# Optimization experiments

Measured on AMD Instinct MI355X. Metric: run time of the kernel, lower is better.

## Reference

```python
import jax, jax.numpy as jnp
import numpy as np

EPS = 1e-8
SMOOTH = 9.0   # lambda_softmax
STEPS = 3      # iteration_step
SLOPE = 0.1    # LeakyReLU slope used by clipped_l2norm


def l2norm(x, axis=-1):
    # matches torch l2norm: x / (sqrt(sum x^2) + eps)
    return x / (jnp.sqrt(jnp.sum(x * x, axis=axis, keepdims=True)) + EPS)


def cos_sim(a, b, axis=-1):
    num = jnp.sum(a * b, axis=axis)
    den = jnp.linalg.norm(a, axis=axis) * jnp.linalg.norm(b, axis=axis)
    return num / jnp.maximum(den, EPS)


def duplicate_mask(cap):
    # same_word logic: cap_k identical to cap_c (off-diagonal). Computed via
    # pairwise squared distances (one GEMM) instead of O(B^2 L d) direct compare.
    B = cap.shape[0]
    flat = cap.reshape(B, -1)
    sq = jnp.sum(flat * flat, axis=1)
    d2 = sq[:, None] + sq[None, :] - 2.0 * (flat @ flat.T)
    return (d2 <= 1e-6) & (~jnp.eye(B, dtype=bool))


def gated(q, a, Wl, bl, Wg, bg):
    cat = jnp.concatenate([q, a], axis=-1)            # (..., 2d)
    lin = jnp.tanh(cat @ Wl.T + bl)
    gate = jax.nn.sigmoid(cat @ Wg.T + bg)
    return q * gate + lin * (1.0 - gate)


def imram_forward(img, cap, W_lt2i, b_lt2i, W_gt2i, b_gt2i,
                  W_li2t, b_li2t, W_gi2t, b_gi2t):
    B, R, D = img.shape
    L = cap.shape[1]
    dup = duplicate_mask(cap)                         # symmetric
    total = jnp.zeros((B, B), img.dtype)              # [caption, image] (training=True transpose)

    # ---- text-to-image: query = caption words, context = image regions ----
    cap_e = jnp.broadcast_to(cap[:, None], (B, B, L, D))   # (cap c, img i, L, D)
    q = cap_e
    for _ in range(STEPS):
        attn = jnp.einsum('ird,cild->cirl', img, q)          # (c,i,R,L)
        attn = l2norm(jax.nn.leaky_relu(attn, SLOPE), axis=-1)   # clipped_l2norm over queryL
        attn = jax.nn.softmax(SMOOTH * attn, axis=2)             # softmax over source regions r
        wc = jnp.einsum('cirl,ird->cild', attn, img)             # weightedContext (c,i,L,D)
        sim = jnp.mean(cos_sim(cap_e, wc, axis=-1), axis=-1)    # (c,i)
        total = total + jnp.where(dup, -1.0, sim)
        q = l2norm(gated(q, wc, W_lt2i, b_lt2i, W_gt2i, b_gt2i), axis=-1)

    # ---- image-to-text: query = image regions, context = caption words ----
    img_e = jnp.broadcast_to(img[None], (B, B, R, D))
    q = img_e
    for _ in range(STEPS):
        attn = jnp.einsum('cld,cird->cilr', cap, q)          # (c,i,L,R)
        attn = l2norm(jax.nn.leaky_relu(attn, SLOPE), axis=-1)   # over queryL (= R)
        attn = jax.nn.softmax(SMOOTH * attn, axis=2)             # over source words l
        wc = jnp.einsum('cilr,cld->cird', attn, cap)             # (c,i,R,D)
        sim = jnp.mean(cos_sim(img_e, wc, axis=-1), axis=-1)
        total = total + jnp.where(dup, -1.0, sim)
        q = l2norm(gated(q, wc, W_li2t, b_li2t, W_gi2t, b_gi2t), axis=-1)

    return total


def setup_inputs() -> dict:
    key = jax.random.key(0)
    ks = jax.random.split(key, 8)
    B, R, L, D = 32, 36, 40, 1024
    img_emb = jax.random.normal(ks[0], (B, R, D), dtype=jnp.float32)
    cap_emb = jax.random.normal(ks[1], (B, L, D), dtype=jnp.float32)
    cap_lens = jax.random.randint(ks[2], (B,), 5, L + 1)
    s = 0.02
    W_lt2i = s * jax.random.normal(ks[3], (D, 2 * D), dtype=jnp.float32)
    W_gt2i = s * jax.random.normal(ks[4], (D, 2 * D), dtype=jnp.float32)
    W_li2t = s * jax.random.normal(ks[5], (D, 2 * D), dtype=jnp.float32)
    W_gi2t = s * jax.random.normal(ks[6], (D, 2 * D), dtype=jnp.float32)
    z = jnp.zeros((D,), jnp.float32)
    return {
        'img_emb': img_emb, 'cap_emb': cap_emb,
        'W_lt2i': W_lt2i, 'b_lt2i': z, 'W_gt2i': W_gt2i, 'b_gt2i': z,
        'W_li2t': W_li2t, 'b_li2t': z, 'W_gi2t': W_gi2t, 'b_gi2t': z,
        'cap_lens': cap_lens,
    }


def reference(img_emb, cap_emb, W_lt2i, b_lt2i, W_gt2i, b_gt2i,
              W_li2t, b_li2t, W_gi2t, b_gi2t, cap_lens):
    # cap_lens is read but never used by the original forward (n_word unused)
    return imram_forward(img_emb, cap_emb, W_lt2i, b_lt2i, W_gt2i, b_gt2i,
                         W_li2t, b_li2t, W_gi2t, b_gi2t)
```

## Files before the change

### kernel.cpp

```cpp
#include <hip/hip_runtime.h>
#include <stdint.h>
#include <math.h>

typedef unsigned short u16;
typedef unsigned int u32;

#define EPSF 1e-8f
#define SMOOTHF 9.0f
#define SLOPEF 0.1f

__device__ __forceinline__ u16 f2bf(float f) {
  union { float f; u32 u; } v; v.f = f;
  u32 u = v.u;
  u32 r = (u + 0x7FFFu + ((u >> 16) & 1u)) >> 16;
  return (u16)r;
}
__device__ __forceinline__ float bf2f(u16 h) {
  union { u32 u; float f; } v; v.u = ((u32)h) << 16;
  return v.f;
}

__device__ __forceinline__ float wave_red_sum(float x) {
#pragma unroll
  for (int off = 32; off; off >>= 1) x += __shfl_xor(x, off, 64);
  return x;
}

__device__ __forceinline__ float block_red_sum(float x) {
  __shared__ float rs[4];
  x = wave_red_sum(x);
  const int lane = threadIdx.x & 63, wv = threadIdx.x >> 6;
  if (lane == 0) rs[wv] = x;
  __syncthreads();
  float r = rs[0] + rs[1] + rs[2] + rs[3];
  __syncthreads();
  return r;
}

__global__ __launch_bounds__(256) void rownorm_kernel(
    const float* __restrict__ cap, const float* __restrict__ img,
    float* __restrict__ capn, float* __restrict__ imgn) {
  const int row = blockIdx.x;
  const float* p; float* o;
  if (row < 1280) { p = cap + (size_t)row * 1024; o = capn + row; }
  else            { p = img + (size_t)(row - 1280) * 1024; o = imgn + (row - 1280); }
  float ss = 0.f;
  for (int d = threadIdx.x; d < 1024; d += 256) { float v = p[d]; ss += v * v; }
  float t = block_red_sum(ss);
  if (threadIdx.x == 0) *o = sqrtf(t);
}

__global__ __launch_bounds__(256) void dup_kernel(
    const float* __restrict__ cap, int* __restrict__ dup) {
  const int b = blockIdx.x;
  const int c = b >> 5, i = b & 31;
  float ss = 0.f;
  if (c != i) {
    const float* A = cap + (size_t)c * 40960;
    const float* B = cap + (size_t)i * 40960;
    for (int e = threadIdx.x; e < 40960; e += 256) { float d = A[e] - B[e]; ss += d * d; }
  }
  float t = block_red_sum(ss);
  if (threadIdx.x == 0) dup[b] = (c != i && t <= 1e-6f) ? 1 : 0;
}

__global__ __launch_bounds__(256) void wconv_kernel(
    const float* __restrict__ Wl, const float* __restrict__ Wg, u16* __restrict__ out) {
  const size_t idx = ((size_t)blockIdx.x * 256 + threadIdx.x) * 4;
  const int n = (int)(idx >> 11);
  const int k = (int)(idx & 2047);
  const float* src = (n & 1) ? &Wg[(size_t)(n >> 1) * 2048 + k] : &Wl[(size_t)(n >> 1) * 2048 + k];
  float4 v = *(const float4*)src;
  ushort4 o;
  o.x = f2bf(v.x); o.y = f2bf(v.y); o.z = f2bf(v.z); o.w = f2bf(v.w);
  *(ushort4*)&out[idx] = o;
}

__global__ __launch_bounds__(256) void bfpad_kernel(
    const float* __restrict__ src, u16* __restrict__ dst, int nrows) {
  const int b = blockIdx.x;
  const int blk = b / 48, r = b - blk * 48;
  u16* orow = dst + (size_t)b * 1024;
  const int tid = threadIdx.x;
  ushort4 o = {0, 0, 0, 0};
  if (r < nrows) {
    const float4 v = *(const float4*)&src[((size_t)blk * nrows + r) * 1024 + tid * 4];
    o.x = f2bf(v.x); o.y = f2bf(v.y); o.z = f2bf(v.z); o.w = f2bf(v.w);
  }
  *(ushort4*)&orow[tid * 4] = o;
}

__global__ __launch_bounds__(256) void ss_kernel(
    const float* __restrict__ src, float* __restrict__ out, int nrows) {
  const int s = blockIdx.x, b = blockIdx.y;
  float* orow = out + ((size_t)b * 48 + s) * 64;
  __shared__ float Ls[1024];
  const int tid = threadIdx.x;
  if (s < nrows)
    *(float4*)&Ls[tid * 4] = *(const float4*)&src[((size_t)b * nrows + s) * 1024 + tid * 4];
  __syncthreads();
  const int s2 = tid >> 2, koff = (tid & 3) * 256;
  float acc = 0.f;
  if (s < nrows && s2 < nrows) {
    const float* r2 = src + ((size_t)b * nrows + s2) * 1024 + koff;
    for (int k = 0; k < 256; k += 4) {
      float4 a = *(const float4*)&Ls[koff + k];
      float4 bb = *(const float4*)&r2[k];
      acc += a.x * bb.x + a.y * bb.y + a.z * bb.z + a.w * bb.w;
    }
  }
  acc += __shfl_xor(acc, 1, 64);
  acc += __shfl_xor(acc, 2, 64);
  if ((tid & 3) == 0) orow[s2] = acc;
}

typedef short bf16x8 __attribute__((ext_vector_type(8)));
typedef float f32x4 __attribute__((ext_vector_type(4)));

#define GLDS(gp, lp)                                                                   \
  __builtin_amdgcn_global_load_lds((const __attribute__((address_space(1))) void*)(gp), \
                                   (__attribute__((address_space(3))) void*)(lp), 16, 0, 0)

__global__ __launch_bounds__(256) void gemm_flex_kernel(
    const u16* __restrict__ A, const u16* __restrict__ B, u16* __restrict__ Cout,
    int koff, int trans) {
  __shared__ u16 As[128 * 32];
  __shared__ u16 Bs[128 * 32];
  const int tid = threadIdx.x;
  const int lane = tid & 63;
  const int wave = tid >> 6;
  const int wm = (wave >> 1) * 64;
  const int wn = (wave & 1) * 64;
  const int bm = blockIdx.x * 128;
  const int bn = blockIdx.y * 128;
  const int lr = lane & 15;
  const int lq = lane >> 4;
  f32x4 acc[4][4] = {};
  const int e0 = tid * 8;
  const int r0 = e0 >> 5;
  const int c0 = e0 & 31;
  const u16* Ag0 = A + (size_t)(bm + r0) * 1024 + c0;
  const u16* Ag1 = A + (size_t)(bm + r0 + 64) * 1024 + c0;
  const u16* Bg0 = B + (size_t)(bn + r0) * 2048 + koff + c0;
  const u16* Bg1 = B + (size_t)(bn + r0 + 64) * 2048 + koff + c0;
  u16* As0 = As + e0; u16* As1 = As + e0 + 2048;
  u16* Bs0 = Bs + e0; u16* Bs1 = Bs + e0 + 2048;
  for (int k0 = 0; k0 < 1024; k0 += 32) {
    GLDS(Ag0 + k0, As0);
    GLDS(Ag1 + k0, As1);
    GLDS(Bg0 + k0, Bs0);
    GLDS(Bg1 + k0, Bs1);
    __syncthreads();
    bf16x8 af[4], bfr[4];
#pragma unroll
    for (int mi = 0; mi < 4; mi++)
      af[mi] = *(const bf16x8*)&As[(wm + mi * 16 + lr) * 32 + lq * 8];
#pragma unroll
    for (int ni = 0; ni < 4; ni++)
      bfr[ni] = *(const bf16x8*)&Bs[(wn + ni * 16 + lr) * 32 + lq * 8];
#pragma unroll
    for (int mi = 0; mi < 4; mi++)
#pragma unroll
      for (int ni = 0; ni < 4; ni++)
        acc[mi][ni] = __builtin_amdgcn_mfma_f32_16x16x32_bf16(af[mi], bfr[ni], acc[mi][ni], 0, 0, 0);
    __syncthreads();
  }
#pragma unroll
  for (int mi = 0; mi < 4; mi++) {
#pragma unroll
    for (int ni = 0; ni < 4; ni++) {
      const int col = bn + wn + ni * 16 + lr;
      const int rowb = bm + wm + mi * 16 + lq * 4;
      if (!trans) {
#pragma unroll
        for (int r = 0; r < 4; r++)
          Cout[(size_t)(rowb + r) * 2048 + col] = f2bf(acc[mi][ni][r]);
      } else {
#pragma unroll
        for (int r = 0; r < 4; r++) {
          const int m = rowb + r;
          const int blk = m / 48, s = m - blk * 48;
          Cout[((size_t)blk * 2048 + col) * 64 + s] = f2bf(acc[mi][ni][r]);
        }
      }
    }
  }
}

__global__ __launch_bounds__(256) void gemm_e_kernel(
    const u16* __restrict__ A, const u16* __restrict__ B, float* __restrict__ C) {
  __shared__ u16 As[128 * 32];
  __shared__ u16 Bs[128 * 32];
  const int tid = threadIdx.x;
  const int lane = tid & 63;
  const int wave = tid >> 6;
  const int wm = (wave >> 1) * 64;
  const int wn = (wave & 1) * 64;
  const int bm = blockIdx.x * 128;
  const int bn = blockIdx.y * 128;
  const int lr = lane & 15;
  const int lq = lane >> 4;
  f32x4 acc[4][4] = {};
  const int e0 = tid * 8;
  const int r0 = e0 >> 5;
  const int c0 = e0 & 31;
  const u16* Ag0 = A + (size_t)(bm + r0) * 1024 + c0;
  const u16* Ag1 = A + (size_t)(bm + r0 + 64) * 1024 + c0;
  const u16* Bg0 = B + (size_t)(bn + r0) * 1024 + c0;
  const u16* Bg1 = B + (size_t)(bn + r0 + 64) * 1024 + c0;
  u16* As0 = As + e0; u16* As1 = As + e0 + 2048;
  u16* Bs0 = Bs + e0; u16* Bs1 = Bs + e0 + 2048;
  for (int k0 = 0; k0 < 1024; k0 += 32) {
    GLDS(Ag0 + k0, As0);
    GLDS(Ag1 + k0, As1);
    GLDS(Bg0 + k0, Bs0);
    GLDS(Bg1 + k0, Bs1);
    __syncthreads();
    bf16x8 af[4], bfr[4];
#pragma unroll
    for (int mi = 0; mi < 4; mi++)
      af[mi] = *(const bf16x8*)&As[(wm + mi * 16 + lr) * 32 + lq * 8];
#pragma unroll
    for (int ni = 0; ni < 4; ni++)
      bfr[ni] = *(const bf16x8*)&Bs[(wn + ni * 16 + lr) * 32 + lq * 8];
#pragma unroll
    for (int mi = 0; mi < 4; mi++)
#pragma unroll
      for (int ni = 0; ni < 4; ni++)
        acc[mi][ni] = __builtin_amdgcn_mfma_f32_16x16x32_bf16(af[mi], bfr[ni], acc[mi][ni], 0, 0, 0);
    __syncthreads();
  }
#pragma unroll
  for (int mi = 0; mi < 4; mi++)
#pragma unroll
    for (int ni = 0; ni < 4; ni++) {
      const int col = bn + wn + ni * 16 + lr;
      const int rowb = bm + wm + mi * 16 + lq * 4;
#pragma unroll
      for (int r = 0; r < 4; r++)
        C[(size_t)(rowb + r) * 1536 + col] = acc[mi][ni][r];
    }
}

template <int STEP, int NQ, int BM>
__global__ __launch_bounds__(512) void wcgate_kernel(
    const u16* __restrict__ attnTg, const u16* __restrict__ q2nd,
    const u16* __restrict__ qref, const u16* __restrict__ SWT,
    const u16* __restrict__ Wcat, const u16* __restrict__ qw0,
    const float* __restrict__ bl, const float* __restrict__ bg,
    u16* __restrict__ Uout, int p0, int swz) {
  constexpr int NT = (STEP == 1) ? 17 : 1;
  constexpr int BUF = (BM + 256) * 64;
  constexpr int WMR = BM / 32;
  constexpr int APASS = BM / 64;
  constexpr int QPASS = BM / 32;
  __shared__ u16 sh[(STEP == 0) ? 73728 : 2 * BUF];
  const int tid = threadIdx.x;
  const int lane = tid & 63;
  const int wave = tid >> 6;
  const int wr = wave >> 2, wc = wave & 3;
  const int wm = wr * (BM / 2), wn = wc * 64;
  const int lr = lane & 15, lq = lane >> 4;
  const int b = blockIdx.y * 8 + blockIdx.x;
  int bmi, bni;
  if (swz) { bmi = (b & 7) + (b >> 6) * 8; bni = (b >> 3) & 7; }
  else     { bmi = blockIdx.y; bni = blockIdx.x; }
  const int bm = bmi * BM;
  const int bn = bni * 256;
  const int sIdx = (p0 + bm / NQ) >> 5;
  f32x4 acc[WMR][4] = {};

  int aoff[APASS]; const u16* asrc0[APASS]; const u16* asrcW[APASS];
  int boff[4]; const u16* bsrc0[4]; const u16* bsrcW[4];
#pragma unroll
  for (int p = 0; p < APASS; p++) {
    const int c = p * 512 + tid;
    const int row = c >> 3, sub = c & 7;
    const int sw = (sub ^ (row & 7)) << 3;
    aoff[p] = c * 8;
    asrc0[p] = attnTg + (size_t)(bm + row) * 64 + sw;
    asrcW[p] = q2nd + (size_t)(bm + row) * 1024 + sw;
  }
#pragma unroll
  for (int p = 0; p < 4; p++) {
    const int c = p * 512 + tid;
    const int row = c >> 3, sub = c & 7;
    const int sw = (sub ^ (row & 7)) << 3;
    boff[p] = c * 8;
    bsrc0[p] = SWT + ((size_t)sIdx * 2048 + bn + row) * 64 + sw;
    bsrcW[p] = Wcat + (size_t)(bn + row) * 2048 + sw;
  }

  u16* const qvS = (STEP == 0) ? sh + 24576 : sh + BUF;
  u16* const qw0S = sh + 40960;
  u16* const stash = sh;

  auto epi_stage = [&]() {
#pragma unroll
    for (int p = 0; p < QPASS; p++) {
      const int c = p * 512 + tid;
      const int row = c >> 4, j = c & 15;
      const u16* src;
      if (STEP == 1) {
        src = qref + (size_t)(bm + row) * 1024 + (bn >> 1) + j * 8;
      } else {
        const int m = bm + row;
        const int pl = m / NQ;
        const int q = m - pl * NQ;
        const int gs = ((p0 + pl) & 31) * 48 + q;
        src = qref + (size_t)gs * 1024 + (bn >> 1) + j * 8;
      }
      GLDS(src, qvS + c * 8);
    }
    if (STEP == 0) {
#pragma unroll
      for (int p = 0; p < 8; p++) {
        const int c = p * 512 + tid;
        const int row = c >> 5, j = c & 31;
        const int m = bm + row;
        const int pl = m / NQ;
        const int q = m - pl * NQ;
        const int gs = ((p0 + pl) & 31) * 48 + q;
        GLDS(qw0 + (size_t)gs * 2048 + bn + j * 8, qw0S + c * 8);
      }
    }
  };

  auto compute = [&](const u16* A, const u16* B) {
#pragma unroll
    for (int kk = 0; kk < 2; kk++) {
      bf16x8 bfv[4];
#pragma unroll
      for (int ni = 0; ni < 4; ni++) {
        const int rb = wn + ni * 16 + lr;
        bfv[ni] = *(const bf16x8*)&B[rb * 64 + ((kk * 32 + lq * 8) ^ ((rb & 7) << 3))];
      }
#pragma unroll
      for (int mi = 0; mi < WMR; mi++) {
        const int ra = wm + mi * 16 + lr;
        const bf16x8 af = *(const bf16x8*)&A[ra * 64 + ((kk * 32 + lq * 8) ^ ((ra & 7) << 3))];
#pragma unroll
        for (int ni = 0; ni < 4; ni++)
          acc[mi][ni] = __builtin_amdgcn_mfma_f32_16x16x32_bf16(af, bfv[ni], acc[mi][ni], 0, 0, 0);
      }
    }
  };

  if constexpr (STEP == 0) {
#pragma unroll
    for (int p = 0; p < APASS; p++) GLDS(asrc0[p], sh + aoff[p]);
#pragma unroll
    for (int p = 0; p < 4; p++) GLDS(bsrc0[p], sh + BM * 64 + boff[p]);
    epi_stage();
    asm volatile("s_waitcnt vmcnt(12)" ::: "memory");
    __builtin_amdgcn_sched_barrier(0);
    __builtin_amdgcn_s_barrier();
    compute(sh, sh + BM * 64);
    __syncthreads();
  } else {
#pragma unroll
    for (int p = 0; p < APASS; p++) GLDS(asrc0[p], sh + aoff[p]);
#pragma unroll
    for (int p = 0; p < 4; p++) GLDS(bsrc0[p], sh + BM * 64 + boff[p]);
    __syncthreads();
#pragma unroll
    for (int tt = 0; tt < NT; ++tt) {
      u16* cur = sh + (tt & 1) * BUF;
      u16* nxt = sh + ((tt & 1) ^ 1) * BUF;
      if (tt < NT - 1) {
#pragma unroll
        for (int p = 0; p < APASS; p++) GLDS(asrcW[p] + tt * 64, nxt + aoff[p]);
#pragma unroll
        for (int p = 0; p < 4; p++) GLDS(bsrcW[p] + tt * 64, nxt + BM * 64 + boff[p]);
      } else {
        epi_stage();
      }
      compute(cur, cur + BM * 64);
      __syncthreads();
    }
  }

  const bool evn = (lane & 1) == 0;
#pragma unroll
  for (int ni = 0; ni < 4; ni++) {
    const int ncol = wn + ni * 16 + lr;
    const int dloc = ncol >> 1;
    const float blv = bl[(bn >> 1) + dloc];
    const float bgv = bg[(bn >> 1) + dloc];
#pragma unroll
    for (int mi = 0; mi < WMR; mi++) {
      const int base = wm + mi * 16 + lq * 4;
#pragma unroll
      for (int rr = 0; rr < 4; rr += 2) {
        const float a0 = acc[mi][ni][rr];
        const float a1 = acc[mi][ni][rr + 1];
        const float o0 = __shfl_xor(a0, 1, 64);
        const float o1 = __shfl_xor(a1, 1, 64);
        float lin2 = (evn ? a0 : o1) + blv;
        float gt = (evn ? o0 : a1) + bgv;
        const int rl = base + rr + (evn ? 0 : 1);
        if constexpr (STEP == 0) {
          const u32 pair = *(const u32*)&qw0S[rl * 256 + dloc * 2];
          lin2 += bf2f((u16)(pair & 0xffffu));
          gt += bf2f((u16)(pair >> 16));
        }
        const float qv = bf2f(qvS[rl * 128 + dloc]);
        lin2 = fminf(fmaxf(lin2, -30.f), 30.f);
        gt = fminf(fmaxf(gt, -30.f), 30.f);
        const float gg = 1.f / (1.f + __expf(-gt));
        const float e2 = __expf(-2.f * lin2);
        const float th = (1.f - e2) / (1.f + e2);
        const float u = qv * gg + th * (1.f - gg);
        stash[rl * 128 + dloc] = f2bf(u);
      }
    }
  }
  __syncthreads();
#pragma unroll
  for (int p = 0; p < QPASS; p++) {
    const int c = p * 512 + tid;
    const int row = c >> 4, j = c & 15;
    *(bf16x8*)(Uout + (size_t)(bm + row) * 1024 + (bn >> 1) + j * 8) =
        *(const bf16x8*)&stash[row * 128 + j * 8];
  }
}

__global__ __launch_bounds__(256) void qnorm_kernel(u16* __restrict__ Q) {
  const int m = blockIdx.x * 4 + (threadIdx.x >> 6);
  const int lane = threadIdx.x & 63;
  u16* p = Q + (size_t)m * 1024;
  float v[16];
  float ss = 0.f;
#pragma unroll
  for (int t = 0; t < 4; t++) {
    ushort4 uv = *(const ushort4*)&p[t * 256 + lane * 4];
    float a = bf2f(uv.x), b = bf2f(uv.y), c = bf2f(uv.z), dd = bf2f(uv.w);
    v[t * 4 + 0] = a; v[t * 4 + 1] = b; v[t * 4 + 2] = c; v[t * 4 + 3] = dd;
    ss += a * a + b * b + c * c + dd * dd;
  }
  ss = wave_red_sum(ss);
  const float inv = 1.f / (sqrtf(ss) + EPSF);
#pragma unroll
  for (int t = 0; t < 4; t++) {
    ushort4 ov;
    ov.x = f2bf(v[t * 4 + 0] * inv); ov.y = f2bf(v[t * 4 + 1] * inv);
    ov.z = f2bf(v[t * 4 + 2] * inv); ov.w = f2bf(v[t * 4 + 3] * inv);
    *(ushort4*)&p[t * 256 + lane * 4] = ov;
  }
}

template <int NS, int NQ>
__global__ __launch_bounds__(256) void attn_step_kernel(
    const u16* __restrict__ Sbf, const float* __restrict__ E,
    const float* __restrict__ SS, const float* __restrict__ refn,
    const u16* __restrict__ qsrc, u16* __restrict__ attnTg,
    const int* __restrict__ dup, float* __restrict__ total,
    int p0, int t2i, int step) {
  constexpr int NQW = NQ / 4;
  const int pl = blockIdx.x;
  const int plg = p0 + pl;
  const int sIdx = plg >> 5, rIdx = plg & 31;
  const int c = t2i ? rIdx : sIdx;
  const int i = t2i ? sIdx : rIdx;
  const int gp = c * 32 + i;
  const u16* Sb = Sbf + (size_t)sIdx * 48 * 1024;
  const float* rn = refn + (size_t)rIdx * NQ;
  const u16* Qb = qsrc + (size_t)pl * NQ * 1024;

  __shared__ float redbuf[9600];
  __shared__ float attnS[2304];
  __shared__ float redcos[48];
  float* Elw = redbuf;
  float* SSl = redbuf + 3120;

  const int tid = threadIdx.x;
  const int lane = tid & 63, wave = tid >> 6;
  const int lr = lane & 15, quad = lane >> 4;

  if (step == 0) {
    for (int e = tid; e < 2304; e += 256) {
      int s, q; float v;
      if (t2i) { s = e / 48; q = e - s * 48; v = E[(size_t)(i * 48 + s) * 1536 + c * 48 + q]; }
      else     { q = e / 48; s = e - q * 48; v = E[(size_t)(i * 48 + q) * 1536 + c * 48 + s]; }
      attnS[s * 48 + q] = v;
    }
  } else {
    f32x4 acc[3][3] = {};
    const int kw = wave * 256;
    const u16* Arow[3]; const u16* Brow[3];
#pragma unroll
    for (int a = 0; a < 3; a++) {
      Arow[a] = Sb + (size_t)(a * 16 + lr) * 1024 + quad * 8;
      Brow[a] = Qb + (size_t)(a * 16 + lr) * 1024 + quad * 8;
    }
    bf16x8 A0[3], B0[3], A1[3], B1[3];
#pragma unroll
    for (int a = 0; a < 3; a++) {
      A0[a] = *(const bf16x8*)(Arow[a] + kw);
      B0[a] = *(const bf16x8*)(Brow[a] + kw);
    }
#pragma unroll
    for (int j = 0; j < 8; j++) {
      if (j < 7) {
        const int kn = kw + (j + 1) * 32;
#pragma unroll
        for (int a = 0; a < 3; a++) {
          A1[a] = *(const bf16x8*)(Arow[a] + kn);
          B1[a] = *(const bf16x8*)(Brow[a] + kn);
        }
      }
#pragma unroll
      for (int a = 0; a < 3; a++)
#pragma unroll
        for (int b = 0; b < 3; b++)
          acc[a][b] = __builtin_amdgcn_mfma_f32_16x16x32_bf16(A0[a], B0[b], acc[a][b], 0, 0, 0);
#pragma unroll
      for (int a = 0; a < 3; a++) { A0[a] = A1[a]; B0[a] = B1[a]; }
    }
    float* myred = redbuf + wave * 2400;
#pragma unroll
    for (int a = 0; a < 3; a++)
#pragma unroll
      for (int b = 0; b < 3; b++) {
        const int col = b * 16 + lr;
        const int row0 = a * 16 + quad * 4;
#pragma unroll
        for (int r = 0; r < 4; r++)
          myred[(row0 + r) * 50 + col] = acc[a][b][r];
      }
    __syncthreads();
#pragma unroll
    for (int t = 0; t < 9; t++) {
      const int e = tid + t * 256;
      const int s = e / 48, q = e - s * 48;
      const int o = s * 50 + q;
      attnS[e] = redbuf[o] + redbuf[2400 + o] + redbuf[4800 + o] + redbuf[7200 + o];
    }
  }
  __syncthreads();
  for (int e = tid; e < 2304; e += 256) {
    int s, q; float v;
    if (t2i) { s = e / 48; q = e - s * 48; v = E[(size_t)(i * 48 + s) * 1536 + c * 48 + q]; }
    else     { q = e / 48; s = e - q * 48; v = E[(size_t)(i * 48 + q) * 1536 + c * 48 + s]; }
    Elw[s * 65 + q] = v;
  }
  for (int e = tid; e < 48 * 64; e += 256) {
    const int s = e >> 6, s2 = e & 63;
    SSl[s * 65 + s2] = SS[((size_t)sIdx * 48 + s) * 64 + s2];
  }
  if (tid < NS) {
    float row[NQ];
    float ss = 0.f;
#pragma unroll
    for (int q = 0; q < NQ; q++) {
      float v = attnS[tid * 48 + q];
      v = (v > 0.f) ? v : SLOPEF * v;
      row[q] = v; ss += v * v;
    }
    const float inv = 1.f / (sqrtf(ss) + EPSF);
#pragma unroll
    for (int q = 0; q < NQ; q++) attnS[tid * 48 + q] = row[q] * inv;
  }
  __syncthreads();
  if (tid < NQ) {
    float mx = -1e30f;
#pragma unroll
    for (int s = 0; s < NS; s++) mx = fmaxf(mx, attnS[s * 48 + tid]);
    float ex[NS]; float sum = 0.f;
#pragma unroll
    for (int s = 0; s < NS; s++) {
      float t = __expf(SMOOTHF * (attnS[s * 48 + tid] - mx));
      ex[s] = t; sum += t;
    }
    const float inv = 1.f / sum;
#pragma unroll
    for (int s = 0; s < NS; s++) attnS[s * 48 + tid] = ex[s] * inv;
  }
  __syncthreads();
  if (step < 2) {
    for (int e = tid; e < NQ * 64; e += 256) {
      const int q = e >> 6, s = e & 63;
      attnTg[((size_t)(pl * NQ + q)) * 64 + s] = (s < 48) ? f2bf(attnS[s * 48 + q]) : (u16)0;
    }
  }
  {
    const int qbase = wave * NQW;
#pragma unroll
    for (int qq = 0; qq < NQW; qq++) {
      const int q = qbase + qq;
      const float a_l = (lane < 48) ? attnS[lane * 48 + q] : 0.f;
      float t = 0.f;
#pragma unroll
      for (int s = 0; s < NS; s++)
        t += attnS[s * 48 + q] * SSl[s * 65 + lane];
      float pssv = wave_red_sum(a_l * t);
      float numv = wave_red_sum(a_l * Elw[lane * 65 + q]);
      if (lane == 0) redcos[q] = numv / fmaxf(rn[q] * sqrtf(pssv), EPSF);
    }
  }
  __syncthreads();
  if (tid == 0) {
    float sim = 0.f;
#pragma unroll
    for (int q = 0; q < NQ; q++) sim += redcos[q];
    sim *= (1.0f / NQ);
    atomicAdd(&total[gp], dup[gp] ? -1.0f : sim);
  }
}

extern "C" void kernel_launch(void* const* d_in, const int* in_sizes, int n_in,
                              void* d_out, int out_size, void* d_ws, size_t ws_size,
                              hipStream_t stream) {
  (void)in_sizes; (void)n_in;
  const float* img = (const float*)d_in[0];
  const float* cap = (const float*)d_in[1];
  const float* W_lt2i = (const float*)d_in[2];
  const float* b_lt2i = (const float*)d_in[3];
  const float* W_gt2i = (const float*)d_in[4];
  const float* b_gt2i = (const float*)d_in[5];
  const float* W_li2t = (const float*)d_in[6];
  const float* b_li2t = (const float*)d_in[7];
  const float* W_gi2t = (const float*)d_in[8];
  const float* b_gi2t = (const float*)d_in[9];
  float* total = (float*)d_out;

  char* ws = (char*)d_ws;
  size_t off = 0;
  auto alloc = [&](size_t b) { void* p = ws + off; off += (b + 255) & ~(size_t)255; return p; };
  u16* Wcat = (u16*)alloc((size_t)2048 * 2048 * 2);
  u16* imgbf = (u16*)alloc((size_t)32 * 48 * 1024 * 2);
  u16* capbf = (u16*)alloc((size_t)32 * 48 * 1024 * 2);
  float* capn = (float*)alloc(1280 * 4);
  float* imgn = (float*)alloc(1152 * 4);
  int* dupb = (int*)alloc(1024 * 4);
  u16* SWT = (u16*)alloc((size_t)32 * 2048 * 64 * 2);
  float* E = (float*)alloc((size_t)1536 * 1536 * 4);
  float* SSi = (float*)alloc((size_t)32 * 48 * 64 * 4);
  float* SSc = (float*)alloc((size_t)32 * 48 * 64 * 4);
  u16* QW0 = (u16*)alloc((size_t)1536 * 2048 * 2);
  const size_t fixed = off;

  static const int cands[6] = {1024, 512, 256, 128, 64, 32};
  int P = 32;
  for (int ci = 0; ci < 6; ci++) {
    const int cand = cands[ci];
    const size_t cA = (((size_t)cand * 40 * 1024 * 2) + 255) & ~(size_t)255;
    const size_t aT = (((size_t)cand * 40 * 64 * 2) + 255) & ~(size_t)255;
    if (fixed + 2 * cA + aT <= ws_size) { P = cand; break; }
  }
  u16* catA = (u16*)alloc((size_t)P * 40 * 1024 * 2);
  u16* catB = (u16*)alloc((size_t)P * 40 * 1024 * 2);
  u16* attnTg = (u16*)alloc((size_t)P * 40 * 64 * 2);

  hipMemsetAsync(d_out, 0, (size_t)out_size * sizeof(float), stream);
  hipMemsetAsync(SWT, 0, (size_t)32 * 2048 * 64 * 2, stream);
  rownorm_kernel<<<dim3(2432), dim3(256), 0, stream>>>(cap, img, capn, imgn);
  dup_kernel<<<dim3(1024), dim3(256), 0, stream>>>(cap, dupb);
  bfpad_kernel<<<dim3(1536), dim3(256), 0, stream>>>(cap, capbf, 40);
  bfpad_kernel<<<dim3(1536), dim3(256), 0, stream>>>(img, imgbf, 36);
  gemm_e_kernel<<<dim3(12, 12), dim3(256), 0, stream>>>(imgbf, capbf, E);
  ss_kernel<<<dim3(48, 32), dim3(256), 0, stream>>>(img, SSi, 36);
  ss_kernel<<<dim3(48, 32), dim3(256), 0, stream>>>(cap, SSc, 40);

  const int nch = 1024 / P;
  for (int dir = 0; dir < 2; dir++) {
    const int t2i = (dir == 0) ? 1 : 0;
    const float* Wl = t2i ? W_lt2i : W_li2t;
    const float* Wg = t2i ? W_gt2i : W_gi2t;
    const float* bl = t2i ? b_lt2i : b_li2t;
    const float* bg = t2i ? b_gt2i : b_gi2t;
    const u16* Sbf = t2i ? imgbf : capbf;
    const u16* Refbf = t2i ? capbf : imgbf;
    const float* SSd = t2i ? SSi : SSc;
    const float* refn = t2i ? capn : imgn;
    const int NQ = t2i ? 40 : 36;
    const int BM1 = t2i ? 256 : 192;
    const int Mrows = P * NQ;
    const int Mt0 = Mrows / 128;
    const int Mt1 = Mrows / BM1;
    const int swz0 = (Mt0 % 8 == 0) ? 1 : 0;
    const int swz1 = (Mt1 % 8 == 0) ? 1 : 0;
    wconv_kernel<<<dim3(4096), dim3(256), 0, stream>>>(Wl, Wg, Wcat);
    gemm_flex_kernel<<<dim3(12, 16), dim3(256), 0, stream>>>(Sbf, Wcat, SWT, 1024, 1);
    gemm_flex_kernel<<<dim3(12, 16), dim3(256), 0, stream>>>(Refbf, Wcat, QW0, 0, 0);
    for (int ch = 0; ch < nch; ch++) {
      const int p0 = ch * P;
      for (int step = 0; step < 3; step++) {
        const u16* qsrc = (step == 1) ? catB : catA;
        if (t2i)
          attn_step_kernel<36, 40><<<dim3(P), dim3(256), 0, stream>>>(
              Sbf, E, SSd, refn, qsrc, attnTg, dupb, total, p0, 1, step);
        else
          attn_step_kernel<40, 36><<<dim3(P), dim3(256), 0, stream>>>(
              Sbf, E, SSd, refn, qsrc, attnTg, dupb, total, p0, 0, step);
        if (step == 0) {
          if (t2i)
            wcgate_kernel<0, 40, 128><<<dim3(8, Mt0), dim3(512), 0, stream>>>(
                attnTg, catA, Refbf, SWT, Wcat, QW0, bl, bg, catB, p0, swz0);
          else
            wcgate_kernel<0, 36, 128><<<dim3(8, Mt0), dim3(512), 0, stream>>>(
                attnTg, catA, Refbf, SWT, Wcat, QW0, bl, bg, catB, p0, swz0);
          qnorm_kernel<<<dim3(Mrows / 4), dim3(256), 0, stream>>>(catB);
        } else if (step == 1) {
          if (t2i)
            wcgate_kernel<1, 40, 256><<<dim3(8, Mt1), dim3(512), 0, stream>>>(
                attnTg, catB, catB, SWT, Wcat, QW0, bl, bg, catA, p0, swz1);
          else
            wcgate_kernel<1, 36, 192><<<dim3(8, Mt1), dim3(512), 0, stream>>>(
                attnTg, catB, catB, SWT, Wcat, QW0, bl, bg, catA, p0, swz1);
          qnorm_kernel<<<dim3(Mrows / 4), dim3(256), 0, stream>>>(catA);
        }
      }
    }
  }
}
```

Before: 1.407 ms.

## Fuse step-0 weighted-context gate GEMM into attention kernel epilogue

The separate step-0 wcgate launch is removed. Its small GEMM (attention weights times precomputed SWT, plus the QW0 term and gating) now runs inside attn_step_kernel, per block, straight from the softmax result held in shared memory. This avoids writing and re-reading attnTg and saves one launch per chunk. The cost is a larger shared-memory footprint in the attention kernel, which may reduce occupancy, and each block has fewer threads (256) for that GEMM.

```diff
diff --git a/kernel.cpp b/kernel.cpp
--- a/kernel.cpp
+++ b/kernel.cpp
@@ -249,12 +249,12 @@
     const u16* __restrict__ Wcat, const u16* __restrict__ qw0,
     const float* __restrict__ bl, const float* __restrict__ bg,
     u16* __restrict__ Uout, int p0, int swz) {
-  constexpr int NT = (STEP == 1) ? 17 : 1;
+  constexpr int NT = 17;
   constexpr int BUF = (BM + 256) * 64;
   constexpr int WMR = BM / 32;
   constexpr int APASS = BM / 64;
   constexpr int QPASS = BM / 32;
-  __shared__ u16 sh[(STEP == 0) ? 73728 : 2 * BUF];
+  __shared__ u16 sh[2 * BUF];
   const int tid = threadIdx.x;
   const int lane = tid & 63;
   const int wave = tid >> 6;
@@ -291,8 +291,7 @@
     bsrcW[p] = Wcat + (size_t)(bn + row) * 2048 + sw;
   }
 
-  u16* const qvS = (STEP == 0) ? sh + 24576 : sh + BUF;
-  u16* const qw0S = sh + 40960;
+  u16* const qvS = sh + BUF;
   u16* const stash = sh;
 
   auto epi_stage = [&]() {
@@ -300,29 +299,7 @@
     for (int p = 0; p < QPASS; p++) {
       const int c = p * 512 + tid;
       const int row = c >> 4, j = c & 15;
-      const u16* src;
-      if (STEP == 1) {
-        src = qref + (size_t)(bm + row) * 1024 + (bn >> 1) + j * 8;
-      } else {
-        const int m = bm + row;
-        const int pl = m / NQ;
-        const int q = m - pl * NQ;
-        const int gs = ((p0 + pl) & 31) * 48 + q;
-        src = qref + (size_t)gs * 1024 + (bn >> 1) + j * 8;
-      }
-      GLDS(src, qvS + c * 8);
-    }
-    if (STEP == 0) {
-#pragma unroll
-      for (int p = 0; p < 8; p++) {
-        const int c = p * 512 + tid;
-        const int row = c >> 5, j = c & 31;
-        const int m = bm + row;
-        const int pl = m / NQ;
-        const int q = m - pl * NQ;
-        const int gs = ((p0 + pl) & 31) * 48 + q;
-        GLDS(qw0 + (size_t)gs * 2048 + bn + j * 8, qw0S + c * 8);
-      }
+      GLDS(qref + (size_t)(bm + row) * 1024 + (bn >> 1) + j * 8, qvS + c * 8);
     }
   };
 
@@ -346,38 +323,25 @@
     }
   };
 
-  if constexpr (STEP == 0) {
-#pragma unroll
-    for (int p = 0; p < APASS; p++) GLDS(asrc0[p], sh + aoff[p]);
-#pragma unroll
-    for (int p = 0; p < 4; p++) GLDS(bsrc0[p], sh + BM * 64 + boff[p]);
-    epi_stage();
-    asm volatile("s_waitcnt vmcnt(12)" ::: "memory");
-    __builtin_amdgcn_sched_barrier(0);
-    __builtin_amdgcn_s_barrier();
-    compute(sh, sh + BM * 64);
+#pragma unroll
+  for (int p = 0; p < APASS; p++) GLDS(asrc0[p], sh + aoff[p]);
+#pragma unroll
+  for (int p = 0; p < 4; p++) GLDS(bsrc0[p], sh + BM * 64 + boff[p]);
+  __syncthreads();
+#pragma unroll
+  for (int tt = 0; tt < NT; ++tt) {
+    u16* cur = sh + (tt & 1) * BUF;
+    u16* nxt = sh + ((tt & 1) ^ 1) * BUF;
+    if (tt < NT - 1) {
+#pragma unroll
+      for (int p = 0; p < APASS; p++) GLDS(asrcW[p] + tt * 64, nxt + aoff[p]);
+#pragma unroll
+      for (int p = 0; p < 4; p++) GLDS(bsrcW[p] + tt * 64, nxt + BM * 64 + boff[p]);
+    } else {
+      epi_stage();
+    }
+    compute(cur, cur + BM * 64);
     __syncthreads();
-  } else {
-#pragma unroll
-    for (int p = 0; p < APASS; p++) GLDS(asrc0[p], sh + aoff[p]);
-#pragma unroll
-    for (int p = 0; p < 4; p++) GLDS(bsrc0[p], sh + BM * 64 + boff[p]);
-    __syncthreads();
-#pragma unroll
-    for (int tt = 0; tt < NT; ++tt) {
-      u16* cur = sh + (tt & 1) * BUF;
-      u16* nxt = sh + ((tt & 1) ^ 1) * BUF;
-      if (tt < NT - 1) {
-#pragma unroll
-        for (int p = 0; p < APASS; p++) GLDS(asrcW[p] + tt * 64, nxt + aoff[p]);
-#pragma unroll
-        for (int p = 0; p < 4; p++) GLDS(bsrcW[p] + tt * 64, nxt + BM * 64 + boff[p]);
-      } else {
-        epi_stage();
-      }
-      compute(cur, cur + BM * 64);
-      __syncthreads();
-    }
   }
 
   const bool evn = (lane & 1) == 0;
@@ -399,11 +363,6 @@
         float lin2 = (evn ? a0 : o1) + blv;
         float gt = (evn ? o0 : a1) + bgv;
         const int rl = base + rr + (evn ? 0 : 1);
-        if constexpr (STEP == 0) {
-          const u32 pair = *(const u32*)&qw0S[rl * 256 + dloc * 2];
-          lin2 += bf2f((u16)(pair & 0xffffu));
-          gt += bf2f((u16)(pair >> 16));
-        }
         const float qv = bf2f(qvS[rl * 128 + dloc]);
         lin2 = fminf(fmaxf(lin2, -30.f), 30.f);
         gt = fminf(fmaxf(gt, -30.f), 30.f);
@@ -455,6 +414,9 @@
     const float* __restrict__ SS, const float* __restrict__ refn,
     const u16* __restrict__ qsrc, u16* __restrict__ attnTg,
     const int* __restrict__ dup, float* __restrict__ total,
+    const u16* __restrict__ SWT, const u16* __restrict__ qw0,
+    const u16* __restrict__ qrefD, const float* __restrict__ bl,
+    const float* __restrict__ bg, u16* __restrict__ Uout,
     int p0, int t2i, int step) {
   constexpr int NQW = NQ / 4;
   const int pl = blockIdx.x;
@@ -467,7 +429,7 @@
   const float* rn = refn + (size_t)rIdx * NQ;
   const u16* Qb = qsrc + (size_t)pl * NQ * 1024;
 
-  __shared__ float redbuf[9600];
+  __shared__ float redbuf[20480];
   __shared__ float attnS[2304];
   __shared__ float redcos[48];
   float* Elw = redbuf;
@@ -577,7 +539,7 @@
     for (int s = 0; s < NS; s++) attnS[s * 48 + tid] = ex[s] * inv;
   }
   __syncthreads();
-  if (step < 2) {
+  if (step == 1) {
     for (int e = tid; e < NQ * 64; e += 256) {
       const int q = e >> 6, s = e & 63;
       attnTg[((size_t)(pl * NQ + q)) * 64 + s] = (s < 48) ? f2bf(attnS[s * 48 + q]) : (u16)0;
@@ -605,6 +567,113 @@
     for (int q = 0; q < NQ; q++) sim += redcos[q];
     sim *= (1.0f / NQ);
     atomicAdd(&total[gp], dup[gp] ? -1.0f : sim);
+  }
+
+  if (step == 0) {
+    u16* pool = (u16*)redbuf;
+    u16* Atile = pool;
+    u16* ustash = pool + 3072;
+    u16* slots[2] = { pool + 6144, pool + 23552 };
+    const int gsb = rIdx * 48;
+
+    auto stageD = [&](int nb, u16* slot) {
+#pragma unroll
+      for (int p = 0; p < 4; p++) {
+        const int cc = p * 256 + tid;
+        const int row = cc >> 3, sub = cc & 7;
+        const int sw = (sub ^ (row & 7)) << 3;
+        GLDS(SWT + ((size_t)sIdx * 2048 + nb * 128 + row) * 64 + sw, slot + cc * 8);
+      }
+#pragma unroll
+      for (int p = 0; p < 2; p++) {
+        const int cc = p * 256 + tid;
+        if (cc < 384) {
+          const int row = cc >> 3, j = cc & 7;
+          GLDS(qrefD + (size_t)(gsb + row) * 1024 + nb * 64 + j * 8, slot + 8192 + cc * 8);
+        }
+      }
+#pragma unroll
+      for (int p = 0; p < 3; p++) {
+        const int cc = p * 256 + tid;
+        const int row = cc >> 4, j = cc & 15;
+        GLDS(qw0 + (size_t)(gsb + row) * 2048 + nb * 128 + j * 8, slot + 11264 + cc * 8);
+      }
+    };
+
+    for (int e = tid; e < 3072; e += 256) {
+      const int q = e >> 6, s = e & 63;
+      const float v = (s < 48) ? attnS[s * 48 + q] : 0.f;
+      Atile[(q << 6) + (s ^ ((q & 7) << 3))] = f2bf(v);
+    }
+    stageD(0, slots[0]);
+    __syncthreads();
+
+    const int wnD = wave * 32;
+    const bool evn = (lane & 1) == 0;
+    for (int nb = 0; nb < 16; ++nb) {
+      u16* cur = slots[nb & 1];
+      if (nb < 15) stageD(nb + 1, slots[(nb + 1) & 1]);
+      const u16* qvC = cur + 8192;
+      const u16* qwC = cur + 11264;
+      f32x4 accD[3][2] = {};
+#pragma unroll
+      for (int kk = 0; kk < 2; kk++) {
+        bf16x8 bfv[2];
+#pragma unroll
+        for (int ni = 0; ni < 2; ni++) {
+          const int rb = wnD + ni * 16 + lr;
+          bfv[ni] = *(const bf16x8*)&cur[rb * 64 + ((kk * 32 + quad * 8) ^ ((rb & 7) << 3))];
+        }
+#pragma unroll
+        for (int mi = 0; mi < 3; mi++) {
+          const int ra = mi * 16 + lr;
+          const bf16x8 af = *(const bf16x8*)&Atile[ra * 64 + ((kk * 32 + quad * 8) ^ ((ra & 7) << 3))];
+#pragma unroll
+          for (int ni = 0; ni < 2; ni++)
+            accD[mi][ni] = __builtin_amdgcn_mfma_f32_16x16x32_bf16(af, bfv[ni], accD[mi][ni], 0, 0, 0);
+        }
+      }
+#pragma unroll
+      for (int ni = 0; ni < 2; ni++) {
+        const int ncol = wnD + ni * 16 + lr;
+        const int dl = ncol >> 1;
+        const int d = nb * 64 + dl;
+        const float blv = bl[d];
+        const float bgv = bg[d];
+#pragma unroll
+        for (int mi = 0; mi < 3; mi++) {
+          const int base = mi * 16 + quad * 4;
+#pragma unroll
+          for (int rr = 0; rr < 4; rr += 2) {
+            const float a0 = accD[mi][ni][rr];
+            const float a1 = accD[mi][ni][rr + 1];
+            const float o0 = __shfl_xor(a0, 1, 64);
+            const float o1 = __shfl_xor(a1, 1, 64);
+            float lin2 = (evn ? a0 : o1) + blv;
+            float gt = (evn ? o0 : a1) + bgv;
+            const int rl = base + rr + (evn ? 0 : 1);
+            const u32 pair = *(const u32*)&qwC[rl * 128 + dl * 2];
+            lin2 += bf2f((u16)(pair & 0xffffu));
+            gt += bf2f((u16)(pair >> 16));
+            const float qv = bf2f(qvC[rl * 64 + dl]);
+            lin2 = fminf(fmaxf(lin2, -30.f), 30.f);
+            gt = fminf(fmaxf(gt, -30.f), 30.f);
+            const float gg = 1.f / (1.f + __expf(-gt));
+            const float e2 = __expf(-2.f * lin2);
+            const float th = (1.f - e2) / (1.f + e2);
+            const float u = qv * gg + th * (1.f - gg);
+            ustash[rl * 64 + dl] = f2bf(u);
+          }
+        }
+      }
+      __syncthreads();
+      for (int e = tid; e < NQ * 8; e += 256) {
+        const int row = e >> 3, j = e & 7;
+        *(bf16x8*)(Uout + (size_t)(pl * NQ + row) * 1024 + nb * 64 + j * 8) =
+            *(const bf16x8*)&ustash[row * 64 + j * 8];
+      }
+      __syncthreads();
+    }
   }
 }
 
@@ -676,9 +745,7 @@
     const int NQ = t2i ? 40 : 36;
     const int BM1 = t2i ? 256 : 192;
     const int Mrows = P * NQ;
-    const int Mt0 = Mrows / 128;
     const int Mt1 = Mrows / BM1;
-    const int swz0 = (Mt0 % 8 == 0) ? 1 : 0;
     const int swz1 = (Mt1 % 8 == 0) ? 1 : 0;
     wconv_kernel<<<dim3(4096), dim3(256), 0, stream>>>(Wl, Wg, Wcat);
     gemm_flex_kernel<<<dim3(12, 16), dim3(256), 0, stream>>>(Sbf, Wcat, SWT, 1024, 1);
@@ -689,17 +756,13 @@
         const u16* qsrc = (step == 1) ? catB : catA;
         if (t2i)
           attn_step_kernel<36, 40><<<dim3(P), dim3(256), 0, stream>>>(
-              Sbf, E, SSd, refn, qsrc, attnTg, dupb, total, p0, 1, step);
+              Sbf, E, SSd, refn, qsrc, attnTg, dupb, total,
+              SWT, QW0, Refbf, bl, bg, catB, p0, 1, step);
         else
           attn_step_kernel<40, 36><<<dim3(P), dim3(256), 0, stream>>>(
-              Sbf, E, SSd, refn, qsrc, attnTg, dupb, total, p0, 0, step);
+              Sbf, E, SSd, refn, qsrc, attnTg, dupb, total,
+              SWT, QW0, Refbf, bl, bg, catB, p0, 0, step);
         if (step == 0) {
-          if (t2i)
-            wcgate_kernel<0, 40, 128><<<dim3(8, Mt0), dim3(512), 0, stream>>>(
-                attnTg, catA, Refbf, SWT, Wcat, QW0, bl, bg, catB, p0, swz0);
-          else
-            wcgate_kernel<0, 36, 128><<<dim3(8, Mt0), dim3(512), 0, stream>>>(
-                attnTg, catA, Refbf, SWT, Wcat, QW0, bl, bg, catB, p0, swz0);
           qnorm_kernel<<<dim3(Mrows / 4), dim3(256), 0, stream>>>(catB);
         } else if (step == 1) {
           if (t2i)
```

Result: slower. 1.718 ms (+22.1%).

## Fold query l2-normalization into attention and gate kernels, drop qnorm pass

Applied to the files above, without the earlier changes.

Removes the separate qnorm kernel, which read and rewrote the whole query buffer after each gated update. Instead, the attention step kernel computes per-row norms of the unnormalized query, divides the attention scores by them, rescales the stored attention, and writes the norms to a small global buffer. The step-1 gate kernel then applies the inverse norm to its accumulators and the query value. This saves a full read-modify-write pass per step, at the cost of extra norm reductions inside the attention kernel and slightly different rounding from working with unnormalized bf16 values.

```diff
diff --git a/kernel.cpp b/kernel.cpp
--- a/kernel.cpp
+++ b/kernel.cpp
@@ -248,7 +248,7 @@
     const u16* __restrict__ qref, const u16* __restrict__ SWT,
     const u16* __restrict__ Wcat, const u16* __restrict__ qw0,
     const float* __restrict__ bl, const float* __restrict__ bg,
-    u16* __restrict__ Uout, int p0, int swz) {
+    const float* __restrict__ normg, u16* __restrict__ Uout, int p0, int swz) {
   constexpr int NT = (STEP == 1) ? 17 : 1;
   constexpr int BUF = (BM + 256) * 64;
   constexpr int WMR = BM / 32;
@@ -396,21 +396,27 @@
         const float a1 = acc[mi][ni][rr + 1];
         const float o0 = __shfl_xor(a0, 1, 64);
         const float o1 = __shfl_xor(a1, 1, 64);
-        float lin2 = (evn ? a0 : o1) + blv;
-        float gt = (evn ? o0 : a1) + bgv;
         const int rl = base + rr + (evn ? 0 : 1);
+        float av = (evn ? a0 : o1);
+        float gv = (evn ? o0 : a1);
+        float qvr = bf2f(qvS[rl * 128 + dloc]);
+        if constexpr (STEP == 1) {
+          const float innv = 1.f / normg[bm + rl];
+          av *= innv; gv *= innv; qvr *= innv;
+        }
+        float lin2 = av + blv;
+        float gt = gv + bgv;
         if constexpr (STEP == 0) {
           const u32 pair = *(const u32*)&qw0S[rl * 256 + dloc * 2];
           lin2 += bf2f((u16)(pair & 0xffffu));
           gt += bf2f((u16)(pair >> 16));
         }
-        const float qv = bf2f(qvS[rl * 128 + dloc]);
         lin2 = fminf(fmaxf(lin2, -30.f), 30.f);
         gt = fminf(fmaxf(gt, -30.f), 30.f);
         const float gg = 1.f / (1.f + __expf(-gt));
         const float e2 = __expf(-2.f * lin2);
         const float th = (1.f - e2) / (1.f + e2);
-        const float u = qv * gg + th * (1.f - gg);
+        const float u = qvr * gg + th * (1.f - gg);
         stash[rl * 128 + dloc] = f2bf(u);
       }
     }
@@ -422,30 +428,6 @@
     const int row = c >> 4, j = c & 15;
     *(bf16x8*)(Uout + (size_t)(bm + row) * 1024 + (bn >> 1) + j * 8) =
         *(const bf16x8*)&stash[row * 128 + j * 8];
-  }
-}
-
-__global__ __launch_bounds__(256) void qnorm_kernel(u16* __restrict__ Q) {
-  const int m = blockIdx.x * 4 + (threadIdx.x >> 6);
-  const int lane = threadIdx.x & 63;
-  u16* p = Q + (size_t)m * 1024;
-  float v[16];
-  float ss = 0.f;
-#pragma unroll
-  for (int t = 0; t < 4; t++) {
-    ushort4 uv = *(const ushort4*)&p[t * 256 + lane * 4];
-    float a = bf2f(uv.x), b = bf2f(uv.y), c = bf2f(uv.z), dd = bf2f(uv.w);
-    v[t * 4 + 0] = a; v[t * 4 + 1] = b; v[t * 4 + 2] = c; v[t * 4 + 3] = dd;
-    ss += a * a + b * b + c * c + dd * dd;
-  }
-  ss = wave_red_sum(ss);
-  const float inv = 1.f / (sqrtf(ss) + EPSF);
-#pragma unroll
-  for (int t = 0; t < 4; t++) {
-    ushort4 ov;
-    ov.x = f2bf(v[t * 4 + 0] * inv); ov.y = f2bf(v[t * 4 + 1] * inv);
-    ov.z = f2bf(v[t * 4 + 2] * inv); ov.w = f2bf(v[t * 4 + 3] * inv);
-    *(ushort4*)&p[t * 256 + lane * 4] = ov;
   }
 }
 
@@ -455,7 +437,7 @@
     const float* __restrict__ SS, const float* __restrict__ refn,
     const u16* __restrict__ qsrc, u16* __restrict__ attnTg,
     const int* __restrict__ dup, float* __restrict__ total,
-    int p0, int t2i, int step) {
+    float* __restrict__ normg, int p0, int t2i, int step) {
   constexpr int NQW = NQ / 4;
   const int pl = blockIdx.x;
   const int plg = p0 + pl;
@@ -470,12 +452,30 @@
   __shared__ float redbuf[9600];
   __shared__ float attnS[2304];
   __shared__ float redcos[48];
+  __shared__ float normP[192];
+  __shared__ float nmS[48];
   float* Elw = redbuf;
   float* SSl = redbuf + 3120;
 
   const int tid = threadIdx.x;
   const int lane = tid & 63, wave = tid >> 6;
   const int lr = lane & 15, quad = lane >> 4;
+
+  if (step > 0) {
+    const int row = tid >> 2, sub = tid & 3;
+    if (row < 48) {
+      float ss = 0.f;
+      if (row < NQ) {
+        const u16* p = Qb + (size_t)row * 1024 + sub * 256;
+        for (int t = 0; t < 32; t++) {
+          bf16x8 v = *(const bf16x8*)(p + t * 8);
+#pragma unroll
+          for (int j = 0; j < 8; j++) { float f = bf2f((u16)v[j]); ss += f * f; }
+        }
+      }
+      normP[row * 4 + sub] = ss;
+    }
+  }
 
   if (step == 0) {
     for (int e = tid; e < 2304; e += 256) {
@@ -534,8 +534,13 @@
       const int e = tid + t * 256;
       const int s = e / 48, q = e - s * 48;
       const int o = s * 50 + q;
-      attnS[e] = redbuf[o] + redbuf[2400 + o] + redbuf[4800 + o] + redbuf[7200 + o];
-    }
+      const float nm = sqrtf(normP[q * 4] + normP[q * 4 + 1] +
+                             normP[q * 4 + 2] + normP[q * 4 + 3]) + EPSF;
+      attnS[e] = (redbuf[o] + redbuf[2400 + o] + redbuf[4800 + o] + redbuf[7200 + o]) / nm;
+    }
+    if (tid < 48)
+      nmS[tid] = sqrtf(normP[tid * 4] + normP[tid * 4 + 1] +
+                       normP[tid * 4 + 2] + normP[tid * 4 + 3]) + EPSF;
   }
   __syncthreads();
   for (int e = tid; e < 2304; e += 256) {
@@ -580,8 +585,11 @@
   if (step < 2) {
     for (int e = tid; e < NQ * 64; e += 256) {
       const int q = e >> 6, s = e & 63;
-      attnTg[((size_t)(pl * NQ + q)) * 64 + s] = (s < 48) ? f2bf(attnS[s * 48 + q]) : (u16)0;
-    }
+      float v = (s < 48) ? attnS[s * 48 + q] : 0.f;
+      if (step == 1) v *= nmS[q];
+      attnTg[((size_t)(pl * NQ + q)) * 64 + s] = (s < 48) ? f2bf(v) : (u16)0;
+    }
+    if (step == 1 && tid < NQ) normg[(size_t)pl * NQ + tid] = nmS[tid];
   }
   {
     const int qbase = wave * NQW;
@@ -646,11 +654,13 @@
     const int cand = cands[ci];
     const size_t cA = (((size_t)cand * 40 * 1024 * 2) + 255) & ~(size_t)255;
     const size_t aT = (((size_t)cand * 40 * 64 * 2) + 255) & ~(size_t)255;
-    if (fixed + 2 * cA + aT <= ws_size) { P = cand; break; }
+    const size_t nG = (((size_t)cand * 40 * 4) + 255) & ~(size_t)255;
+    if (fixed + 2 * cA + aT + nG <= ws_size) { P = cand; break; }
   }
   u16* catA = (u16*)alloc((size_t)P * 40 * 1024 * 2);
   u16* catB = (u16*)alloc((size_t)P * 40 * 1024 * 2);
   u16* attnTg = (u16*)alloc((size_t)P * 40 * 64 * 2);
+  float* normg = (float*)alloc((size_t)P * 40 * 4);
 
   hipMemsetAsync(d_out, 0, (size_t)out_size * sizeof(float), stream);
   hipMemsetAsync(SWT, 0, (size_t)32 * 2048 * 64 * 2, stream);
@@ -689,26 +699,24 @@
         const u16* qsrc = (step == 1) ? catB : catA;
         if (t2i)
           attn_step_kernel<36, 40><<<dim3(P), dim3(256), 0, stream>>>(
-              Sbf, E, SSd, refn, qsrc, attnTg, dupb, total, p0, 1, step);
+              Sbf, E, SSd, refn, qsrc, attnTg, dupb, total, normg, p0, 1, step);
         else
           attn_step_kernel<40, 36><<<dim3(P), dim3(256), 0, stream>>>(
-              Sbf, E, SSd, refn, qsrc, attnTg, dupb, total, p0, 0, step);
+              Sbf, E, SSd, refn, qsrc, attnTg, dupb, total, normg, p0, 0, step);
         if (step == 0) {
           if (t2i)
             wcgate_kernel<0, 40, 128><<<dim3(8, Mt0), dim3(512), 0, stream>>>(
-                attnTg, catA, Refbf, SWT, Wcat, QW0, bl, bg, catB, p0, swz0);
+                attnTg, catA, Refbf, SWT, Wcat, QW0, bl, bg, normg, catB, p0, swz0);
           else
             wcgate_kernel<0, 36, 128><<<dim3(8, Mt0), dim3(512), 0, stream>>>(
-                attnTg, catA, Refbf, SWT, Wcat, QW0, bl, bg, catB, p0, swz0);
-          qnorm_kernel<<<dim3(Mrows / 4), dim3(256), 0, stream>>>(catB);
+                attnTg, catA, Refbf, SWT, Wcat, QW0, bl, bg, normg, catB, p0, swz0);
         } else if (step == 1) {
           if (t2i)
             wcgate_kernel<1, 40, 256><<<dim3(8, Mt1), dim3(512), 0, stream>>>(
-                attnTg, catB, catB, SWT, Wcat, QW0, bl, bg, catA, p0, swz1);
+                attnTg, catB, catB, SWT, Wcat, QW0, bl, bg, normg, catA, p0, swz1);
           else
             wcgate_kernel<1, 36, 192><<<dim3(8, Mt1), dim3(512), 0, stream>>>(
-                attnTg, catB, catB, SWT, Wcat, QW0, bl, bg, catA, p0, swz1);
-          qnorm_kernel<<<dim3(Mrows / 4), dim3(256), 0, stream>>>(catA);
+                attnTg, catB, catB, SWT, Wcat, QW0, bl, bg, normg, catA, p0, swz1);
         }
       }
     }
```

Measured after the change: 1.417 ms. No clear change (+0.7%).
